# Optimization experiments

Hardware: AMD Instinct MI355X
Metric: run time of the kernel (lower is better)

Reference implementation:

```python
import jax, jax.numpy as jnp
import numpy as np

B, IN, OUT, E, H, K = 8192, 1024, 256, 16, 512, 3
EPS = 1e-10


def setup_inputs() -> dict:
    key = jax.random.key(0)
    ks = jax.random.split(key, 5)
    scaled = lambda k, shape, fan: jax.random.normal(k, shape, jnp.float32) / np.sqrt(fan)
    return {
        "x": jax.random.normal(ks[0], (B, IN), jnp.float32),
        # torch init is zeros for w_gate (degenerate ties); use small random for a meaningful reference
        "w_gate": jax.random.normal(ks[1], (IN, E), jnp.float32) * 0.02,
        "W1": scaled(ks[2], (E, IN, H), IN),
        "b1": jnp.zeros((E, H), jnp.float32),
        "W2": scaled(ks[3], (E, H, OUT), H),
        "b2": jnp.zeros((E, OUT), jnp.float32),
    }


def _cv_squared(v):
    # torch .var() is unbiased (ddof=1)
    return jnp.var(v, ddof=1) / (jnp.mean(v) ** 2 + EPS)


def reference(x, w_gate, W1, b1, W2, b2):
    # --- top-k gating (eval mode: clean logits, no noise) ---
    logits = x @ w_gate                                   # [B, E]
    top_vals, top_idx = jax.lax.top_k(logits, K)          # [B, K]
    top_gates = jax.nn.softmax(top_vals, axis=-1)         # softmax over selected k
    rows = jnp.arange(logits.shape[0])[:, None]
    gates = jnp.zeros_like(logits).at[rows, top_idx].set(top_gates)  # sparse gates [B, E]

    # --- load-balancing loss ---
    importance = gates.sum(0)
    load = (gates > 0).sum(0).astype(jnp.float32)         # _gates_to_load (eval path)
    loss = _cv_squared(importance) + _cv_squared(load)

    # --- experts (MLP stand-in; dense compute, sparse combine via zero gates) ---
    h = jax.nn.relu(jnp.einsum('bi,eih->beh', x, W1) + b1)  # [B, E, H]
    expert_out = jnp.einsum('beh,eho->beo', h, W2) + b2     # [B, E, OUT]

    # combine: equivalent to SparseDispatcher gather/split/scatter-add with gate weighting
    y = jnp.einsum('be,beo->bo', gates, expert_out)         # [B, OUT]
    return y, loss
```

## Files before the change

### kernel.cpp

```cpp
#include <hip/hip_runtime.h>

#define B_ 8192
#define IN_ 1024
#define OUT_ 256
#define E_ 16
#define KTOP 3
#define H_ 512
#define MAXSLOTS 26624
#define NTILES 208
#define HBLK 16
#define GBLK 2048

typedef __bf16 bf16;
typedef __bf16 bf16x4 __attribute__((ext_vector_type(4)));
typedef __bf16 bf16x8 __attribute__((ext_vector_type(8)));
typedef float f32x4 __attribute__((ext_vector_type(4)));

__device__ __forceinline__ void async16(const bf16* g, bf16* l) {
    __builtin_amdgcn_global_load_lds(
        (const __attribute__((address_space(1))) void*)g,
        (__attribute__((address_space(3))) void*)l,
        16, 0, 0);
}

__global__ __launch_bounds__(256) void k_stage1(
    const float* __restrict__ x, const float* __restrict__ wg,
    const float* __restrict__ W1, const float* __restrict__ W2,
    bf16* __restrict__ xbf, int* __restrict__ top_idx, float* __restrict__ top_gate,
    int* __restrict__ partial,
    bf16* __restrict__ w1t, bf16* __restrict__ w2t,
    int* __restrict__ row_ids, bf16* __restrict__ zero_row, int* __restrict__ tile_expert) {
    __shared__ __align__(16) float smem[5140];
    int bx = blockIdx.x;
    int t = threadIdx.x;
    if (bx < GBLK) {
        int* lcnt = (int*)(smem + 5124);
        int lane = t & 63;
        int row = bx * 4 + (t >> 6);
        if (t < 16) lcnt[t] = 0;
        float acc[16];
#pragma unroll
        for (int e = 0; e < 16; e++) acc[e] = 0.f;
        const float4* x4p = (const float4*)(x + (size_t)row * IN_);
        float4* swg4 = (float4*)smem;
        for (int q = 0; q < 4; q++) {
            const float4* src = (const float4*)(wg + q * 4096);
#pragma unroll
            for (int i = 0; i < 4; i++) {
                int f = i * 256 + t;
                swg4[(f >> 2) * 5 + (f & 3)] = src[f];
            }
            __syncthreads();
            float4 xv = x4p[q * 64 + lane];
            bf16x4 xb;
            xb[0] = (bf16)xv.x; xb[1] = (bf16)xv.y; xb[2] = (bf16)xv.z; xb[3] = (bf16)xv.w;
            *(bf16x4*)(xbf + (size_t)row * IN_ + (q * 64 + lane) * 4) = xb;
            float xs[4] = {xv.x, xv.y, xv.z, xv.w};
#pragma unroll
            for (int i = 0; i < 4; i++) {
                int r = lane * 4 + i;
#pragma unroll
                for (int e4 = 0; e4 < 4; e4++) {
                    float4 wv = swg4[r * 5 + e4];
                    acc[e4 * 4 + 0] += xs[i] * wv.x;
                    acc[e4 * 4 + 1] += xs[i] * wv.y;
                    acc[e4 * 4 + 2] += xs[i] * wv.z;
                    acc[e4 * 4 + 3] += xs[i] * wv.w;
                }
            }
            __syncthreads();
        }
#pragma unroll
        for (int e = 0; e < 16; e++) {
#pragma unroll
            for (int s = 32; s > 0; s >>= 1) acc[e] += __shfl_xor(acc[e], s, 64);
        }
        if (lane == 0) {
            float v[16];
#pragma unroll
            for (int e = 0; e < 16; e++) v[e] = acc[e];
            int idx[KTOP];
            float val[KTOP];
#pragma unroll
            for (int k = 0; k < KTOP; k++) {
                int best = 0;
                float bv = v[0];
                for (int e = 1; e < 16; e++) {
                    if (v[e] > bv) { bv = v[e]; best = e; }
                }
                idx[k] = best; val[k] = bv; v[best] = -1e30f;
            }
            float e1 = __expf(val[1] - val[0]);
            float e2 = __expf(val[2] - val[0]);
            float inv = 1.f / (1.f + e1 + e2);
            float g[KTOP] = {inv, e1 * inv, e2 * inv};
#pragma unroll
            for (int k = 0; k < KTOP; k++) {
                top_idx[row * KTOP + k] = idx[k];
                top_gate[row * KTOP + k] = g[k];
                atomicAdd(&lcnt[idx[k]], 1);
            }
        }
        __syncthreads();
        if (t < 16) partial[bx * 16 + t] = lcnt[t];
        return;
    }
    if (bx >= 4608) {
        if (bx < 4712) {
            row_ids[(bx - 4608) * 256 + t] = -1;
        } else {
#pragma unroll
            for (int i = 0; i < 4; i++) zero_row[t * 4 + i] = (bf16)0.f;
            if (t < NTILES) tile_expert[t] = -1;
        }
        return;
    }
    float (*tile)[65] = (float(*)[65])smem;
    const float* in; bf16* out; int Kd, Nd, e, tk, tn;
    if (bx < 4096) {
        int b1x = bx - 2048;
        in = W1; out = w1t; Kd = IN_; Nd = H_;
        e = b1x >> 7; int tt = b1x & 127; tk = tt >> 3; tn = tt & 7;
    } else {
        int b2x = bx - 4096;
        in = W2; out = w2t; Kd = H_; Nd = OUT_;
        e = b2x >> 5; int tt = b2x & 31; tk = tt >> 2; tn = tt & 3;
    }
    int r = t >> 6, c = t & 63;
    const float* src = in + ((size_t)e * Kd + tk * 64) * Nd + (size_t)tn * 64;
#pragma unroll
    for (int i = 0; i < 16; i++) {
        int rr = r + i * 4;
        tile[rr][c] = src[(size_t)rr * Nd + c];
    }
    __syncthreads();
    bf16* dst = out + ((size_t)e * Nd + tn * 64) * Kd + (size_t)tk * 64;
#pragma unroll
    for (int i = 0; i < 16; i++) {
        int rr = r + i * 4;
        dst[(size_t)rr * Kd + c] = (bf16)tile[c][rr];
    }
}

__global__ __launch_bounds__(256) void k_scatterscan(
    const int* __restrict__ top_idx, const float* __restrict__ top_gate,
    const int* __restrict__ partial,
    int* __restrict__ counts, int* __restrict__ tile_expert,
    int* __restrict__ row_ids, int* __restrict__ rowslot,
    float* __restrict__ partial_imp) {
    __shared__ int segsum[16][16];
    __shared__ int tote[16];
    __shared__ int sbase[16];
    __shared__ int lcnt[16];
    __shared__ float limp[16];
    int t = threadIdx.x;
    int blk = blockIdx.x;
    int e = t & 15, seg = t >> 4;
    int s = 0;
    for (int i = 0; i < 128; i++) s += partial[(seg * 128 + i) * 16 + e];
    segsum[seg][e] = s;
    if (t < 16) { lcnt[t] = 0; limp[t] = 0.f; }
    __syncthreads();
    if (t < 16) {
        int total = 0, pre = 0;
        for (int sg = 0; sg < 16; sg++) {
            int v = segsum[sg][t];
            total += v;
            if (sg < blk) pre += v;
        }
        tote[t] = total;
        segsum[0][t] = pre;
    }
    __syncthreads();
    if (t < 16) {
        int off = 0;
        for (int ee = 0; ee < 16; ee++) {
            if (ee == t) break;
            off += (tote[ee] + 127) & ~127;
        }
        sbase[t] = off + segsum[0][t];
        if (blk == 0) {
            counts[t] = tote[t];
            int pd = (tote[t] + 127) & ~127;
            for (int tt = off >> 7; tt < (off + pd) >> 7; ++tt) tile_expert[tt] = t;
        }
    }
    __syncthreads();
#pragma unroll
    for (int j = 0; j < 6; j++) {
        int gid = blk * 1536 + j * 256 + t;
        int ee = top_idx[gid];
        float g = top_gate[gid];
        int rank = atomicAdd(&lcnt[ee], 1);
        atomicAdd(&limp[ee], g);
        int slot = sbase[ee] + rank;
        row_ids[slot] = gid / KTOP;
        rowslot[gid] = slot;
    }
    __syncthreads();
    if (t < 16) partial_imp[blk * 16 + t] = limp[t];
}

__global__ __launch_bounds__(512) void k_fused(
    const bf16* __restrict__ xbf, const bf16* __restrict__ w1t,
    const float* __restrict__ b1, const bf16* __restrict__ w2t,
    const float* __restrict__ b2, const int* __restrict__ row_ids,
    const int* __restrict__ tile_expert, const bf16* __restrict__ zero_row,
    bf16* __restrict__ eout) {
    int e = tile_expert[blockIdx.x];
    if (e < 0) return;
    int slot_base = blockIdx.x * 128;
    __shared__ __align__(16) bf16 smem[57344];
    bf16* hs  = smem;
    bf16* As  = smem + 32768;
    bf16* Bs1 = smem + 40960;
    bf16* Bs2 = smem + 32768;
    int t = threadIdx.x;
    int rmod = (t >> 3) & 7;
    int cglob = (t & 7) ^ rmod;
    const bf16* gA[2];
#pragma unroll
    for (int j = 0; j < 2; j++) {
        int m = j * 64 + (t >> 3);
        int rid = row_ids[slot_base + m];
        gA[j] = ((rid >= 0) ? xbf + (size_t)rid * IN_ : zero_row) + cglob * 8;
    }
    const bf16* gB1[4];
#pragma unroll
    for (int j = 0; j < 4; j++) {
        int m = j * 64 + (t >> 3);
        gB1[j] = w1t + ((size_t)e * H_ + m) * IN_ + cglob * 8;
    }
    const bf16* gB2[4];
#pragma unroll
    for (int j = 0; j < 4; j++) {
        int m = j * 64 + (t >> 3);
        gB2[j] = w2t + ((size_t)e * OUT_ + m) * H_ + cglob * 8;
    }
    int w = t >> 6, lane = t & 63;
    int wm = (w & 1) * 64, wn = (w >> 1) * 64;
    int lm = lane & 15, lq = lane >> 4;
    f32x4 acc2[4][4] = {};
    for (int c = 0; c < 2; c++) {
        f32x4 acc1[4][4] = {};
        for (int k0 = 0; k0 < IN_; k0 += 64) {
#pragma unroll
            for (int j = 0; j < 2; j++) async16(gA[j] + k0, As + (j * 512 + t) * 8);
#pragma unroll
            for (int j = 0; j < 4; j++)
                async16(gB1[j] + (size_t)c * (256 * IN_) + k0, Bs1 + (j * 512 + t) * 8);
            __syncthreads();
            const bf16x8* Av = (const bf16x8*)As;
            const bf16x8* Bv = (const bf16x8*)Bs1;
#pragma unroll
            for (int ks = 0; ks < 2; ks++) {
                int kc = ks * 4 + lq;
                bf16x8 af[4], bfv[4];
#pragma unroll
                for (int i = 0; i < 4; i++) {
                    int row = wm + i * 16 + lm;
                    af[i] = Av[row * 8 + (kc ^ (row & 7))];
                }
#pragma unroll
                for (int i = 0; i < 4; i++) {
                    int row = wn + i * 16 + lm;
                    bfv[i] = Bv[row * 8 + (kc ^ (row & 7))];
                }
#pragma unroll
                for (int mi = 0; mi < 4; mi++)
#pragma unroll
                    for (int ni = 0; ni < 4; ni++)
                        acc1[mi][ni] = __builtin_amdgcn_mfma_f32_16x16x32_bf16(af[mi], bfv[ni], acc1[mi][ni], 0, 0, 0);
            }
            __syncthreads();
        }
        const float* b1c = b1 + e * H_ + c * 256;
#pragma unroll
        for (int mi = 0; mi < 4; mi++) {
#pragma unroll
            for (int ni = 0; ni < 4; ni++) {
                int col = wn + ni * 16 + lm;
                float bias = b1c[col];
#pragma unroll
                for (int r = 0; r < 4; r++) {
                    int row = wm + mi * 16 + lq * 4 + r;
                    float v = acc1[mi][ni][r] + bias;
                    v = v > 0.f ? v : 0.f;
                    hs[row * 256 + (((col >> 3) ^ (row & 7)) << 3) + (col & 7)] = (bf16)v;
                }
            }
        }
        __syncthreads();
        for (int s = 0; s < 4; s++) {
#pragma unroll
            for (int j = 0; j < 4; j++)
                async16(gB2[j] + c * 256 + s * 64, Bs2 + (j * 512 + t) * 8);
            __syncthreads();
            const bf16x8* Hv = (const bf16x8*)hs;
            const bf16x8* B2v = (const bf16x8*)Bs2;
#pragma unroll
            for (int ks = 0; ks < 2; ks++) {
                int kc = ks * 4 + lq;
                bf16x8 af[4], bfv[4];
#pragma unroll
                for (int i = 0; i < 4; i++) {
                    int row = wm + i * 16 + lm;
                    af[i] = Hv[row * 32 + ((s * 8 + kc) ^ (row & 7))];
                }
#pragma unroll
                for (int i = 0; i < 4; i++) {
                    int row = wn + i * 16 + lm;
                    bfv[i] = B2v[row * 8 + (kc ^ (row & 7))];
                }
#pragma unroll
                for (int mi = 0; mi < 4; mi++)
#pragma unroll
                    for (int ni = 0; ni < 4; ni++)
                        acc2[mi][ni] = __builtin_amdgcn_mfma_f32_16x16x32_bf16(af[mi], bfv[ni], acc2[mi][ni], 0, 0, 0);
            }
            __syncthreads();
        }
    }
#pragma unroll
    for (int mi = 0; mi < 4; mi++) {
#pragma unroll
        for (int ni = 0; ni < 4; ni++) {
            int colg = wn + ni * 16 + lm;
            float bias = b2[e * OUT_ + colg];
#pragma unroll
            for (int r = 0; r < 4; r++) {
                int rowl = wm + mi * 16 + lq * 4 + r;
                eout[(size_t)(slot_base + rowl) * OUT_ + colg] = (bf16)(acc2[mi][ni][r] + bias);
            }
        }
    }
}

__global__ __launch_bounds__(256) void k_combine(
    const bf16* __restrict__ eout, const int* __restrict__ rowslot,
    const float* __restrict__ top_gate, float* __restrict__ y,
    const float* __restrict__ partial_imp, const int* __restrict__ counts,
    float* __restrict__ loss_out) {
    int t = threadIdx.x;
    if (blockIdx.x == B_ / 4) {
        __shared__ float imp[16];
        if (t < 16) {
            float s = 0.f;
#pragma unroll
            for (int b = 0; b < HBLK; b++) s += partial_imp[b * 16 + t];
            imp[t] = s;
        }
        __syncthreads();
        if (t == 0) {
            float si = 0.f, sl = 0.f;
            for (int e = 0; e < E_; e++) { si += imp[e]; sl += (float)counts[e]; }
            float mi_ = si / (float)E_, ml_ = sl / (float)E_;
            float vi = 0.f, vl = 0.f;
            for (int e = 0; e < E_; e++) {
                float d = imp[e] - mi_; vi += d * d;
                float d2 = (float)counts[e] - ml_; vl += d2 * d2;
            }
            vi /= (float)(E_ - 1); vl /= (float)(E_ - 1);
            *loss_out = vi / (mi_ * mi_ + 1e-10f) + vl / (ml_ * ml_ + 1e-10f);
        }
        return;
    }
    int b = blockIdx.x * 4 + (t >> 6);
    int lane = t & 63;
    int s0 = rowslot[b * 3], s1 = rowslot[b * 3 + 1], s2 = rowslot[b * 3 + 2];
    float g0 = top_gate[b * 3], g1 = top_gate[b * 3 + 1], g2 = top_gate[b * 3 + 2];
    bf16x4 v0 = *(const bf16x4*)(eout + (size_t)s0 * OUT_ + lane * 4);
    bf16x4 v1 = *(const bf16x4*)(eout + (size_t)s1 * OUT_ + lane * 4);
    bf16x4 v2 = *(const bf16x4*)(eout + (size_t)s2 * OUT_ + lane * 4);
    float4 r;
    r.x = g0 * (float)v0[0] + g1 * (float)v1[0] + g2 * (float)v2[0];
    r.y = g0 * (float)v0[1] + g1 * (float)v1[1] + g2 * (float)v2[1];
    r.z = g0 * (float)v0[2] + g1 * (float)v1[2] + g2 * (float)v2[2];
    r.w = g0 * (float)v0[3] + g1 * (float)v1[3] + g2 * (float)v2[3];
    ((float4*)y)[(size_t)b * 64 + lane] = r;
}

extern "C" void kernel_launch(void* const* d_in, const int* in_sizes, int n_in,
                              void* d_out, int out_size, void* d_ws, size_t ws_size,
                              hipStream_t stream) {
    (void)in_sizes; (void)n_in; (void)out_size; (void)ws_size;
    const float* x = (const float*)d_in[0];
    const float* wgate = (const float*)d_in[1];
    const float* W1 = (const float*)d_in[2];
    const float* b1 = (const float*)d_in[3];
    const float* W2 = (const float*)d_in[4];
    const float* b2 = (const float*)d_in[5];
    float* y = (float*)d_out;

    char* p = (char*)d_ws;
    auto alloc = [&](size_t bytes) {
        char* q = p;
        p += (bytes + 255) & ~(size_t)255;
        return q;
    };
    bf16* xbf = (bf16*)alloc((size_t)B_ * IN_ * 2);
    bf16* w1t = (bf16*)alloc((size_t)E_ * H_ * IN_ * 2);
    bf16* w2t = (bf16*)alloc((size_t)E_ * OUT_ * H_ * 2);
    bf16* eout = (bf16*)alloc((size_t)MAXSLOTS * OUT_ * 2);
    int* row_ids = (int*)alloc((size_t)MAXSLOTS * 4);
    int* rowslot = (int*)alloc((size_t)B_ * KTOP * 4);
    int* top_idx = (int*)alloc((size_t)B_ * KTOP * 4);
    float* top_gate = (float*)alloc((size_t)B_ * KTOP * 4);
    int* counts = (int*)alloc(E_ * 4);
    int* partial = (int*)alloc((size_t)GBLK * E_ * 4);
    float* partial_imp = (float*)alloc(HBLK * E_ * 4);
    int* tile_expert = (int*)alloc(NTILES * 4);
    bf16* zero_row = (bf16*)alloc(IN_ * 2);

    k_stage1<<<dim3(4713), dim3(256), 0, stream>>>(
        x, wgate, W1, W2, xbf, top_idx, top_gate, partial, w1t, w2t,
        row_ids, zero_row, tile_expert);
    k_scatterscan<<<dim3(HBLK), dim3(256), 0, stream>>>(
        top_idx, top_gate, partial, counts, tile_expert, row_ids, rowslot, partial_imp);
    k_fused<<<dim3(NTILES), dim3(512), 0, stream>>>(
        xbf, w1t, b1, w2t, b2, row_ids, tile_expert, zero_row, eout);
    k_combine<<<dim3(B_ / 4 + 1), dim3(256), 0, stream>>>(
        eout, rowslot, top_gate, y, partial_imp, counts, y + (size_t)B_ * OUT_);
}
```

Baseline: 217.1 us.

## Double-buffer LDS stages to overlap async loads with MFMA compute

Enlarges the shared-memory buffer so the fused expert kernel keeps two ping-pong stage buffers. The next K-slice of x/W1, or the next W2 slice, is issued with async global-to-LDS loads while the current slice is being computed. Prefetch also crosses phase boundaries, from GEMM1 into GEMM2 and from GEMM2 back into the next GEMM1 chunk. This aims to hide global-load latency that was previously exposed before each compute step. The cost is more LDS per block and a correctness dependence on the remaining barriers correctly separating buffer reuse.

```diff
diff --git a/kernel.cpp b/kernel.cpp
--- a/kernel.cpp
+++ b/kernel.cpp
@@ -210,11 +210,10 @@
     int e = tile_expert[blockIdx.x];
     if (e < 0) return;
     int slot_base = blockIdx.x * 128;
-    __shared__ __align__(16) bf16 smem[57344];
-    bf16* hs  = smem;
-    bf16* As  = smem + 32768;
-    bf16* Bs1 = smem + 40960;
-    bf16* Bs2 = smem + 32768;
+    __shared__ __align__(16) bf16 smem[81920];
+    bf16* hs = smem;
+    bf16* P  = smem + 32768;
+    const int PB = 24576;
     int t = threadIdx.x;
     int rmod = (t >> 3) & 7;
     int cglob = (t & 7) ^ rmod;
@@ -240,18 +239,33 @@
     int w = t >> 6, lane = t & 63;
     int wm = (w & 1) * 64, wn = (w >> 1) * 64;
     int lm = lane & 15, lq = lane >> 4;
+
+    auto stage1 = [&](int p, int c, int k0) {
+        bf16* as  = P + p * PB;
+        bf16* b1s = as + 8192;
+#pragma unroll
+        for (int j = 0; j < 2; j++) async16(gA[j] + k0, as + (j * 512 + t) * 8);
+#pragma unroll
+        for (int j = 0; j < 4; j++)
+            async16(gB1[j] + (size_t)c * (256 * IN_) + k0, b1s + (j * 512 + t) * 8);
+    };
+    auto stage2 = [&](int q, int c, int s) {
+        bf16* b2s = P + q * PB;
+#pragma unroll
+        for (int j = 0; j < 4; j++) async16(gB2[j] + c * 256 + s * 64, b2s + (j * 512 + t) * 8);
+    };
+
     f32x4 acc2[4][4] = {};
+    stage1(0, 0, 0);
+    __syncthreads();
     for (int c = 0; c < 2; c++) {
         f32x4 acc1[4][4] = {};
-        for (int k0 = 0; k0 < IN_; k0 += 64) {
-#pragma unroll
-            for (int j = 0; j < 2; j++) async16(gA[j] + k0, As + (j * 512 + t) * 8);
-#pragma unroll
-            for (int j = 0; j < 4; j++)
-                async16(gB1[j] + (size_t)c * (256 * IN_) + k0, Bs1 + (j * 512 + t) * 8);
-            __syncthreads();
-            const bf16x8* Av = (const bf16x8*)As;
-            const bf16x8* Bv = (const bf16x8*)Bs1;
+        for (int k = 0; k < 16; k++) {
+            if (k < 15) stage1((k + 1) & 1, c, (k + 1) * 64);
+            else        stage2(0, c, 0);
+            int p = k & 1;
+            const bf16x8* Av = (const bf16x8*)(P + p * PB);
+            const bf16x8* Bv = (const bf16x8*)(P + p * PB + 8192);
 #pragma unroll
             for (int ks = 0; ks < 2; ks++) {
                 int kc = ks * 4 + lq;
@@ -292,12 +306,11 @@
         }
         __syncthreads();
         for (int s = 0; s < 4; s++) {
-#pragma unroll
-            for (int j = 0; j < 4; j++)
-                async16(gB2[j] + c * 256 + s * 64, Bs2 + (j * 512 + t) * 8);
-            __syncthreads();
-            const bf16x8* Hv = (const bf16x8*)hs;
-            const bf16x8* B2v = (const bf16x8*)Bs2;
+            if (s < 3)      stage2((s + 1) & 1, c, s + 1);
+            else if (c == 0) stage1(0, 1, 0);
+            int q = s & 1;
+            const bf16x8* Hv  = (const bf16x8*)hs;
+            const bf16x8* B2v = (const bf16x8*)(P + q * PB);
 #pragma unroll
             for (int ks = 0; ks < 2; ks++) {
                 int kc = ks * 4 + lq;
```

Result: faster. 204.9 us (-5.6%).

## Triple-buffer fused expert MLP pipeline and batch gating rows per block

Applied to the files above, without the earlier changes.

The fused expert kernel moves from synchronous per-step loads to a three-buffer async pipeline with BK=32. It waits on vmcnt counters with a single barrier per step and prefetches the W2 stage while GEMM1 is still finishing. Biases and swizzled LDS indices are hoisted into registers. The gating stage now processes 16 rows per block with a transposed w_gate loaded into LDS once, which cuts block count and weight reloads at the cost of more registers and LDS. stageG2 issues a duplicate async load to pad the vmcnt accounting, which adds redundant traffic.

```diff
diff --git a/kernel.cpp b/kernel.cpp
--- a/kernel.cpp
+++ b/kernel.cpp
@@ -9,7 +9,7 @@
 #define MAXSLOTS 26624
 #define NTILES 208
 #define HBLK 16
-#define GBLK 2048
+#define GBLK 512
 
 typedef __bf16 bf16;
 typedef __bf16 bf16x4 __attribute__((ext_vector_type(4)));
@@ -30,84 +30,104 @@
     int* __restrict__ partial,
     bf16* __restrict__ w1t, bf16* __restrict__ w2t,
     int* __restrict__ row_ids, bf16* __restrict__ zero_row, int* __restrict__ tile_expert) {
-    __shared__ __align__(16) float smem[5140];
+    __shared__ __align__(16) float smem[16448];
+    __shared__ int lcnt[16];
     int bx = blockIdx.x;
     int t = threadIdx.x;
     if (bx < GBLK) {
-        int* lcnt = (int*)(smem + 5124);
-        int lane = t & 63;
-        int row = bx * 4 + (t >> 6);
+        float4* swgT4 = (float4*)smem;
+        const float4* wg4 = (const float4*)wg;
         if (t < 16) lcnt[t] = 0;
-        float acc[16];
-#pragma unroll
-        for (int e = 0; e < 16; e++) acc[e] = 0.f;
-        const float4* x4p = (const float4*)(x + (size_t)row * IN_);
-        float4* swg4 = (float4*)smem;
-        for (int q = 0; q < 4; q++) {
-            const float4* src = (const float4*)(wg + q * 4096);
-#pragma unroll
-            for (int i = 0; i < 4; i++) {
-                int f = i * 256 + t;
-                swg4[(f >> 2) * 5 + (f & 3)] = src[f];
-            }
-            __syncthreads();
-            float4 xv = x4p[q * 64 + lane];
-            bf16x4 xb;
-            xb[0] = (bf16)xv.x; xb[1] = (bf16)xv.y; xb[2] = (bf16)xv.z; xb[3] = (bf16)xv.w;
-            *(bf16x4*)(xbf + (size_t)row * IN_ + (q * 64 + lane) * 4) = xb;
-            float xs[4] = {xv.x, xv.y, xv.z, xv.w};
-#pragma unroll
-            for (int i = 0; i < 4; i++) {
-                int r = lane * 4 + i;
-#pragma unroll
-                for (int e4 = 0; e4 < 4; e4++) {
-                    float4 wv = swg4[r * 5 + e4];
-                    acc[e4 * 4 + 0] += xs[i] * wv.x;
-                    acc[e4 * 4 + 1] += xs[i] * wv.y;
-                    acc[e4 * 4 + 2] += xs[i] * wv.z;
-                    acc[e4 * 4 + 3] += xs[i] * wv.w;
+#pragma unroll
+        for (int i = 0; i < 16; i++) {
+            int p = (t & 3) * 4 + ((t >> 2) & 3);
+            int slot = i * 16 + (t >> 4);
+            swgT4[p * 257 + slot] = wg4[i * 256 + t];
+        }
+        __syncthreads();
+        int wv = t >> 6, lane = t & 63;
+#pragma unroll
+        for (int pr = 0; pr < 2; ++pr) {
+            int row = bx * 16 + wv * 4 + pr * 2;
+            const float4* xra = (const float4*)(x + (size_t)row * IN_);
+            const float4* xrb = (const float4*)(x + (size_t)(row + 1) * IN_);
+            float4 xa[4], xb4[4];
+#pragma unroll
+            for (int q = 0; q < 4; q++) { xa[q] = xra[lane + 64 * q]; xb4[q] = xrb[lane + 64 * q]; }
+#pragma unroll
+            for (int q = 0; q < 4; q++) {
+                bf16x4 ca, cb;
+                ca[0] = (bf16)xa[q].x; ca[1] = (bf16)xa[q].y; ca[2] = (bf16)xa[q].z; ca[3] = (bf16)xa[q].w;
+                cb[0] = (bf16)xb4[q].x; cb[1] = (bf16)xb4[q].y; cb[2] = (bf16)xb4[q].z; cb[3] = (bf16)xb4[q].w;
+                *(bf16x4*)(xbf + (size_t)row * IN_ + (size_t)(lane + 64 * q) * 4) = ca;
+                *(bf16x4*)(xbf + (size_t)(row + 1) * IN_ + (size_t)(lane + 64 * q) * 4) = cb;
+            }
+            float acca[16], accb[16];
+#pragma unroll
+            for (int e = 0; e < 16; e++) { acca[e] = 0.f; accb[e] = 0.f; }
+#pragma unroll
+            for (int q = 0; q < 4; q++) {
+                float sa[4] = {xa[q].x, xa[q].y, xa[q].z, xa[q].w};
+                float sb[4] = {xb4[q].x, xb4[q].y, xb4[q].z, xb4[q].w};
+#pragma unroll
+                for (int jj = 0; jj < 4; jj++) {
+#pragma unroll
+                    for (int e4 = 0; e4 < 4; e4++) {
+                        float4 w4 = swgT4[(e4 * 4 + jj) * 257 + lane + 64 * q];
+                        acca[e4 * 4 + 0] += sa[jj] * w4.x;
+                        acca[e4 * 4 + 1] += sa[jj] * w4.y;
+                        acca[e4 * 4 + 2] += sa[jj] * w4.z;
+                        acca[e4 * 4 + 3] += sa[jj] * w4.w;
+                        accb[e4 * 4 + 0] += sb[jj] * w4.x;
+                        accb[e4 * 4 + 1] += sb[jj] * w4.y;
+                        accb[e4 * 4 + 2] += sb[jj] * w4.z;
+                        accb[e4 * 4 + 3] += sb[jj] * w4.w;
+                    }
                 }
             }
-            __syncthreads();
-        }
-#pragma unroll
-        for (int e = 0; e < 16; e++) {
-#pragma unroll
-            for (int s = 32; s > 0; s >>= 1) acc[e] += __shfl_xor(acc[e], s, 64);
-        }
-        if (lane == 0) {
-            float v[16];
-#pragma unroll
-            for (int e = 0; e < 16; e++) v[e] = acc[e];
-            int idx[KTOP];
-            float val[KTOP];
-#pragma unroll
-            for (int k = 0; k < KTOP; k++) {
-                int best = 0;
-                float bv = v[0];
-                for (int e = 1; e < 16; e++) {
-                    if (v[e] > bv) { bv = v[e]; best = e; }
+#pragma unroll
+            for (int e = 0; e < 16; e++) {
+#pragma unroll
+                for (int s = 32; s > 0; s >>= 1) {
+                    acca[e] += __shfl_xor(acca[e], s, 64);
+                    accb[e] += __shfl_xor(accb[e], s, 64);
                 }
-                idx[k] = best; val[k] = bv; v[best] = -1e30f;
-            }
-            float e1 = __expf(val[1] - val[0]);
-            float e2 = __expf(val[2] - val[0]);
-            float inv = 1.f / (1.f + e1 + e2);
-            float g[KTOP] = {inv, e1 * inv, e2 * inv};
-#pragma unroll
-            for (int k = 0; k < KTOP; k++) {
-                top_idx[row * KTOP + k] = idx[k];
-                top_gate[row * KTOP + k] = g[k];
-                atomicAdd(&lcnt[idx[k]], 1);
+            }
+            if (lane < 2) {
+                float v[16];
+#pragma unroll
+                for (int e = 0; e < 16; e++) v[e] = lane ? accb[e] : acca[e];
+                int rsel = row + lane;
+                int idx[KTOP];
+                float val[KTOP];
+#pragma unroll
+                for (int k = 0; k < KTOP; k++) {
+                    int best = 0;
+                    float bv = v[0];
+                    for (int e = 1; e < 16; e++) {
+                        if (v[e] > bv) { bv = v[e]; best = e; }
+                    }
+                    idx[k] = best; val[k] = bv; v[best] = -1e30f;
+                }
+                float e1 = __expf(val[1] - val[0]);
+                float e2 = __expf(val[2] - val[0]);
+                float inv = 1.f / (1.f + e1 + e2);
+                float g[KTOP] = {inv, e1 * inv, e2 * inv};
+#pragma unroll
+                for (int k = 0; k < KTOP; k++) {
+                    top_idx[rsel * KTOP + k] = idx[k];
+                    top_gate[rsel * KTOP + k] = g[k];
+                    atomicAdd(&lcnt[idx[k]], 1);
+                }
             }
         }
         __syncthreads();
         if (t < 16) partial[bx * 16 + t] = lcnt[t];
         return;
     }
-    if (bx >= 4608) {
-        if (bx < 4712) {
-            row_ids[(bx - 4608) * 256 + t] = -1;
+    if (bx >= 3072) {
+        if (bx < 3176) {
+            row_ids[(bx - 3072) * 256 + t] = -1;
         } else {
 #pragma unroll
             for (int i = 0; i < 4; i++) zero_row[t * 4 + i] = (bf16)0.f;
@@ -117,12 +137,12 @@
     }
     float (*tile)[65] = (float(*)[65])smem;
     const float* in; bf16* out; int Kd, Nd, e, tk, tn;
-    if (bx < 4096) {
-        int b1x = bx - 2048;
+    if (bx < 2560) {
+        int b1x = bx - 512;
         in = W1; out = w1t; Kd = IN_; Nd = H_;
         e = b1x >> 7; int tt = b1x & 127; tk = tt >> 3; tn = tt & 7;
     } else {
-        int b2x = bx - 4096;
+        int b2x = bx - 2560;
         in = W2; out = w2t; Kd = H_; Nd = OUT_;
         e = b2x >> 5; int tt = b2x & 31; tk = tt >> 2; tn = tt & 3;
     }
@@ -157,7 +177,8 @@
     int blk = blockIdx.x;
     int e = t & 15, seg = t >> 4;
     int s = 0;
-    for (int i = 0; i < 128; i++) s += partial[(seg * 128 + i) * 16 + e];
+#pragma unroll
+    for (int i = 0; i < GBLK / 16; i++) s += partial[(seg * (GBLK / 16) + i) * 16 + e];
     segsum[seg][e] = s;
     if (t < 16) { lcnt[t] = 0; limp[t] = 0.f; }
     __syncthreads();
@@ -201,6 +222,7 @@
     if (t < 16) partial_imp[blk * 16 + t] = limp[t];
 }
 
+#define VWAIT(N) asm volatile("s_waitcnt vmcnt(" #N ")" ::: "memory")
 __global__ __launch_bounds__(512) void k_fused(
     const bf16* __restrict__ xbf, const bf16* __restrict__ w1t,
     const float* __restrict__ b1, const bf16* __restrict__ w2t,
@@ -210,77 +232,95 @@
     int e = tile_expert[blockIdx.x];
     if (e < 0) return;
     int slot_base = blockIdx.x * 128;
-    __shared__ __align__(16) bf16 smem[57344];
-    bf16* hs  = smem;
-    bf16* As  = smem + 32768;
-    bf16* Bs1 = smem + 40960;
-    bf16* Bs2 = smem + 32768;
+    __shared__ __align__(16) bf16 smem[69632];
+    bf16* hs = smem;
+    bf16* pb0 = smem + 32768;
+    bf16* pb1 = smem + 32768 + 12288;
+    bf16* pb2 = smem + 32768 + 24576;
     int t = threadIdx.x;
-    int rmod = (t >> 3) & 7;
-    int cglob = (t & 7) ^ rmod;
-    const bf16* gA[2];
+    int cg = (t & 3) ^ ((t >> 3) & 3);
+    int rid = row_ids[slot_base + (t >> 2)];
+    const bf16* gA = ((rid >= 0) ? xbf + (size_t)rid * IN_ : zero_row) + cg * 8;
+    const bf16* gB1[2];
+    const bf16* gB2[2];
 #pragma unroll
     for (int j = 0; j < 2; j++) {
-        int m = j * 64 + (t >> 3);
-        int rid = row_ids[slot_base + m];
-        gA[j] = ((rid >= 0) ? xbf + (size_t)rid * IN_ : zero_row) + cglob * 8;
-    }
-    const bf16* gB1[4];
-#pragma unroll
-    for (int j = 0; j < 4; j++) {
-        int m = j * 64 + (t >> 3);
-        gB1[j] = w1t + ((size_t)e * H_ + m) * IN_ + cglob * 8;
-    }
-    const bf16* gB2[4];
-#pragma unroll
-    for (int j = 0; j < 4; j++) {
-        int m = j * 64 + (t >> 3);
-        gB2[j] = w2t + ((size_t)e * OUT_ + m) * H_ + cglob * 8;
+        int m = j * 128 + (t >> 2);
+        gB1[j] = w1t + ((size_t)e * H_ + m) * IN_ + cg * 8;
+        gB2[j] = w2t + ((size_t)e * OUT_ + m) * H_ + cg * 8;
     }
     int w = t >> 6, lane = t & 63;
     int wm = (w & 1) * 64, wn = (w >> 1) * 64;
     int lm = lane & 15, lq = lane >> 4;
+    int aidx[4], bidx[4], hrow[4], hx[4];
+#pragma unroll
+    for (int i = 0; i < 4; i++) {
+        int ra = wm + i * 16 + lm;
+        int rb = wn + i * 16 + lm;
+        aidx[i] = ra * 4 + (lq ^ ((ra >> 1) & 3));
+        bidx[i] = rb * 4 + (lq ^ ((rb >> 1) & 3));
+        hrow[i] = ra * 32;
+        hx[i] = ra & 7;
+    }
+    float rbias1[2][4], rbias2[4];
+#pragma unroll
+    for (int c2 = 0; c2 < 2; ++c2)
+#pragma unroll
+        for (int ni = 0; ni < 4; ++ni) rbias1[c2][ni] = b1[e * H_ + c2 * 256 + wn + ni * 16 + lm];
+#pragma unroll
+    for (int ni = 0; ni < 4; ++ni) rbias2[ni] = b2[e * OUT_ + wn + ni * 16 + lm];
+#pragma unroll
+    for (int c2 = 0; c2 < 2; ++c2)
+#pragma unroll
+        for (int ni = 0; ni < 4; ++ni) asm volatile("" : "+v"(rbias1[c2][ni]));
+#pragma unroll
+    for (int ni = 0; ni < 4; ++ni) asm volatile("" : "+v"(rbias2[ni]));
+
+    auto stageG1 = [&](bf16* buf, int c, int k) {
+        async16(gA + k * 32, buf + t * 8);
+        async16(gB1[0] + (size_t)c * (256 * IN_) + k * 32, buf + 4096 + t * 8);
+        async16(gB1[1] + (size_t)c * (256 * IN_) + k * 32, buf + 4096 + (512 + t) * 8);
+    };
+    auto stageG2 = [&](bf16* buf, int c, int s) {
+        const bf16* p0 = gB2[0] + c * 256 + s * 32;
+        async16(p0, buf + t * 8);
+        async16(gB2[1] + c * 256 + s * 32, buf + (512 + t) * 8);
+        async16(p0, buf + t * 8);
+    };
+
     f32x4 acc2[4][4] = {};
-    for (int c = 0; c < 2; c++) {
+    bf16 *bufA = pb0, *bufB = pb1, *bufC = pb2;
+    stageG1(bufA, 0, 0);
+    stageG1(bufB, 0, 1);
+#pragma unroll
+    for (int c = 0; c < 2; ++c) {
         f32x4 acc1[4][4] = {};
-        for (int k0 = 0; k0 < IN_; k0 += 64) {
-#pragma unroll
-            for (int j = 0; j < 2; j++) async16(gA[j] + k0, As + (j * 512 + t) * 8);
-#pragma unroll
-            for (int j = 0; j < 4; j++)
-                async16(gB1[j] + (size_t)c * (256 * IN_) + k0, Bs1 + (j * 512 + t) * 8);
-            __syncthreads();
-            const bf16x8* Av = (const bf16x8*)As;
-            const bf16x8* Bv = (const bf16x8*)Bs1;
-#pragma unroll
-            for (int ks = 0; ks < 2; ks++) {
-                int kc = ks * 4 + lq;
-                bf16x8 af[4], bfv[4];
-#pragma unroll
-                for (int i = 0; i < 4; i++) {
-                    int row = wm + i * 16 + lm;
-                    af[i] = Av[row * 8 + (kc ^ (row & 7))];
-                }
-#pragma unroll
-                for (int i = 0; i < 4; i++) {
-                    int row = wn + i * 16 + lm;
-                    bfv[i] = Bv[row * 8 + (kc ^ (row & 7))];
-                }
-#pragma unroll
-                for (int mi = 0; mi < 4; mi++)
-#pragma unroll
-                    for (int ni = 0; ni < 4; ni++)
-                        acc1[mi][ni] = __builtin_amdgcn_mfma_f32_16x16x32_bf16(af[mi], bfv[ni], acc1[mi][ni], 0, 0, 0);
-            }
-            __syncthreads();
-        }
-        const float* b1c = b1 + e * H_ + c * 256;
+        for (int k = 0; k < 32; ++k) {
+            VWAIT(3);
+            __builtin_amdgcn_s_barrier();
+            __builtin_amdgcn_sched_barrier(0);
+            const bf16x8* Av = (const bf16x8*)bufA;
+            const bf16x8* Bv = (const bf16x8*)(bufA + 4096);
+            bf16x8 af[4], bfv[4];
+#pragma unroll
+            for (int i = 0; i < 4; i++) af[i] = Av[aidx[i]];
+#pragma unroll
+            for (int i = 0; i < 4; i++) bfv[i] = Bv[bidx[i]];
+#pragma unroll
+            for (int mi = 0; mi < 4; mi++)
+#pragma unroll
+                for (int ni = 0; ni < 4; ni++)
+                    acc1[mi][ni] = __builtin_amdgcn_mfma_f32_16x16x32_bf16(af[mi], bfv[ni], acc1[mi][ni], 0, 0, 0);
+            if (k < 30) stageG1(bufC, c, k + 2);
+            else        stageG2(bufC, c, k - 30);
+            bf16* tmpb = bufA; bufA = bufB; bufB = bufC; bufC = tmpb;
+        }
 #pragma unroll
         for (int mi = 0; mi < 4; mi++) {
 #pragma unroll
             for (int ni = 0; ni < 4; ni++) {
                 int col = wn + ni * 16 + lm;
-                float bias = b1c[col];
+                float bias = rbias1[c][ni];
 #pragma unroll
                 for (int r = 0; r < 4; r++) {
                     int row = wm + mi * 16 + lq * 4 + r;
@@ -290,35 +330,27 @@
                 }
             }
         }
-        __syncthreads();
-        for (int s = 0; s < 4; s++) {
-#pragma unroll
-            for (int j = 0; j < 4; j++)
-                async16(gB2[j] + c * 256 + s * 64, Bs2 + (j * 512 + t) * 8);
-            __syncthreads();
+        asm volatile("s_waitcnt lgkmcnt(0)" ::: "memory");
+#pragma unroll
+        for (int s = 0; s < 8; ++s) {
+            if (c == 1 && s == 7) { VWAIT(0); } else { VWAIT(3); }
+            __builtin_amdgcn_s_barrier();
+            __builtin_amdgcn_sched_barrier(0);
             const bf16x8* Hv = (const bf16x8*)hs;
-            const bf16x8* B2v = (const bf16x8*)Bs2;
-#pragma unroll
-            for (int ks = 0; ks < 2; ks++) {
-                int kc = ks * 4 + lq;
-                bf16x8 af[4], bfv[4];
-#pragma unroll
-                for (int i = 0; i < 4; i++) {
-                    int row = wm + i * 16 + lm;
-                    af[i] = Hv[row * 32 + ((s * 8 + kc) ^ (row & 7))];
-                }
-#pragma unroll
-                for (int i = 0; i < 4; i++) {
-                    int row = wn + i * 16 + lm;
-                    bfv[i] = B2v[row * 8 + (kc ^ (row & 7))];
-                }
-#pragma unroll
-                for (int mi = 0; mi < 4; mi++)
-#pragma unroll
-                    for (int ni = 0; ni < 4; ni++)
-                        acc2[mi][ni] = __builtin_amdgcn_mfma_f32_16x16x32_bf16(af[mi], bfv[ni], acc2[mi][ni], 0, 0, 0);
-            }
-            __syncthreads();
+            const bf16x8* B2v = (const bf16x8*)bufA;
+            bf16x8 af[4], bfv[4];
+#pragma unroll
+            for (int i = 0; i < 4; i++) af[i] = Hv[hrow[i] + ((s * 4 + lq) ^ hx[i])];
+#pragma unroll
+            for (int i = 0; i < 4; i++) bfv[i] = B2v[bidx[i]];
+#pragma unroll
+            for (int mi = 0; mi < 4; mi++)
+#pragma unroll
+                for (int ni = 0; ni < 4; ni++)
+                    acc2[mi][ni] = __builtin_amdgcn_mfma_f32_16x16x32_bf16(af[mi], bfv[ni], acc2[mi][ni], 0, 0, 0);
+            if (s < 6)       stageG2(bufC, c, s + 2);
+            else if (c == 0) stageG1(bufC, 1, s - 6);
+            bf16* tmpb = bufA; bufA = bufB; bufB = bufC; bufC = tmpb;
         }
     }
 #pragma unroll
@@ -326,7 +358,7 @@
 #pragma unroll
         for (int ni = 0; ni < 4; ni++) {
             int colg = wn + ni * 16 + lm;
-            float bias = b2[e * OUT_ + colg];
+            float bias = rbias2[ni];
 #pragma unroll
             for (int r = 0; r < 4; r++) {
                 int rowl = wm + mi * 16 + lq * 4 + r;
@@ -412,7 +444,7 @@
     int* tile_expert = (int*)alloc(NTILES * 4);
     bf16* zero_row = (bf16*)alloc(IN_ * 2);
 
-    k_stage1<<<dim3(4713), dim3(256), 0, stream>>>(
+    k_stage1<<<dim3(3177), dim3(256), 0, stream>>>(
         x, wgate, W1, W2, xbf, top_idx, top_gate, partial, w1t, w2t,
         row_ids, zero_row, tile_expert);
     k_scatterscan<<<dim3(HBLK), dim3(256), 0, stream>>>(
```

New measurement: 186.3 us. 1.17x faster.
